# Kernel tuning notes

Hardware: AMD Instinct MI355X
Metric: run time of the kernel (lower is better)

The kernel has to match this reference:

```python
import jax, jax.numpy as jnp
import numpy as np
from jax import lax

# shifts generated by _generate_shifts(kernel_size=3): (s1, s2) pairs with
# (s1, s2) >= (0, 0) lexicographically, excluding (0, 0)
SHIFTS = [(0, 1), (1, -1), (1, 0), (1, 1)]


def conv2d_same(x, w, b):
    # x: (B, C_in, H, W), w: (C_out, C_in, kH, kW), b: (C_out,)
    y = lax.conv_general_dilated(
        x, w, window_strides=(1, 1), padding='SAME',
        dimension_numbers=('NCHW', 'OIHW', 'NCHW'))
    return y + b[None, :, None, None]


def setup_inputs() -> dict:
    key = jax.random.key(0)
    k1, k2, k3, k4, k5 = jax.random.split(key, 5)
    B, C_in, C_out, H, W, K = 8, 64, 64, 256, 256, 3
    fan = C_in * K * K
    return {
        'x': jax.random.normal(k1, (B, C_in, H, W), dtype=jnp.float32),
        'w1': jax.random.normal(k2, (C_out, C_in, K, K), dtype=jnp.float32) / np.sqrt(fan),
        'b1': jax.random.normal(k3, (C_out,), dtype=jnp.float32) * 0.01,
        'w2': jax.random.normal(k4, (C_out, C_in, K, K), dtype=jnp.float32) / np.sqrt(fan),
        'b2': jax.random.normal(k5, (C_out,), dtype=jnp.float32) * 0.01,
    }


def reference(x, w1, b1, w2, b2):
    linear_term = conv2d_same(x, w1, b1)
    # torch.roll(x, shifts=(shift_y, shift_x), dims=(2,3)) with
    # circular_shift(x, s1, s2) -> shift_x=s1, shift_y=s2.
    # conv2 is linear, so sum_i conv2(prod_i) == conv2(sum_i prod_i)
    # with the bias added once per shift.
    quad_in = jnp.zeros_like(x)
    for s1, s2 in SHIFTS:
        x_shifted = jnp.roll(x, shift=(s2, s1), axis=(2, 3))
        quad_in = quad_in + jnp.clip(x * x_shifted, -1.0, 1.0)
    quadratic_term = conv2d_same(quad_in, w2, b2 * float(len(SHIFTS)))
    return linear_term + quadratic_term
```

## Files before the change

### kernel.cpp

```cpp
#include <hip/hip_runtime.h>
#include <stdint.h>


typedef short s16x8 __attribute__((ext_vector_type(8)));
typedef float f32x4 __attribute__((ext_vector_type(4)));

__device__ __forceinline__ float clip1(float v) { return fminf(fmaxf(v, -1.f), 1.f); }

__device__ __forceinline__ unsigned short f2bf(float f) {
    union { float f; unsigned u; } v; v.f = f;
    unsigned u = v.u;
    return (unsigned short)((u + 0x7fffu + ((u >> 16) & 1u)) >> 16);
}

__device__ __forceinline__ float bf2f(unsigned short u) {
    union { unsigned v; float f; } t; t.v = ((unsigned)u) << 16; return t.f;
}

__global__ void prep_w(const float* __restrict__ w1, const float* __restrict__ w2,
                       unsigned short* __restrict__ Wb) {
    int idx = blockIdx.x * 256 + threadIdx.x;
    int kk = idx % 96;
    int rest = idx / 96;
    int co = rest & 63; rest >>= 6;
    int cc = rest & 3;
    int kh = rest >> 2;
    int kw = kk >> 5;
    int cci = kk & 31;
    int c2 = cc * 32 + cci;
    const float* src = (c2 < 64) ? w1 : w2;
    int ci = c2 & 63;
    Wb[idx] = f2bf(src[((co * 64 + ci) * 3 + kh) * 3 + kw]);
}

__global__ __launch_bounds__(512, 1) void prep_u2(const float* __restrict__ x,
                                                  unsigned short* __restrict__ U) {
    __shared__ unsigned short X[3][64][268];
    int bid = blockIdx.x;
    int bh = ((bid & 7) << 8) + (bid >> 3);
    int b = bh >> 8, h = bh & 255;
    int tid = threadIdx.x;

    for (int it = 0; it < 24; ++it) {
        int idx = tid + (it << 9);
        int w4 = idx & 63;
        int c  = (idx >> 6) & 63;
        int r  = idx >> 12;
        int gr = (h + r + 255) & 255;
        const float4 v = *(const float4*)(x + (((size_t)(b * 64 + c)) << 16)
                                            + (gr << 8) + (w4 << 2));
        ushort4 p;
        p.x = f2bf(v.x); p.y = f2bf(v.y); p.z = f2bf(v.z); p.w = f2bf(v.w);
        *(ushort4*)&X[r][c][w4 << 2] = p;
    }
    __syncthreads();

    int c  = tid & 63;
    int wv = tid >> 6;
    int p0 = wv << 5;
    int pm0 = (p0 + 255) & 255;
    float pxc = bf2f(X[1][c][pm0]);
    float pxu = bf2f(X[0][c][pm0]);
    float pxd = bf2f(X[2][c][pm0]);
    size_t base = ((size_t)bh) << 8;
#pragma unroll 4
    for (int i = 0; i < 32; ++i) {
        int p = p0 + i;
        unsigned short xcb = X[1][c][p];
        float xc = bf2f(xcb);
        float xu = bf2f(X[0][c][p]);
        float xd = bf2f(X[2][c][p]);
        float q = clip1(xc * xu) + clip1(xc * pxd) + clip1(xc * pxc) + clip1(xc * pxu);
        size_t po = (base + p) << 7;
        U[po + c]      = xcb;
        U[po + 64 + c] = f2bf(q);
        pxc = xc; pxu = xu; pxd = xd;
    }
}

__global__ __launch_bounds__(512, 4) void conv5(
        const unsigned short* __restrict__ U,
        const unsigned short* __restrict__ Wb,
        const float* __restrict__ b1, const float* __restrict__ b2,
        float* __restrict__ out) {
    __shared__ unsigned short Alds[3][64][104];
    __shared__ unsigned short Ib[2][130][40];

    int bid = blockIdx.x;
    int logical = ((bid & 7) << 7) + (bid >> 3);
    int b = logical >> 7;
    int rem = logical & 127;
    int h0 = (rem >> 1) << 2;
    int whalf = rem & 1;
    int w0 = whalf << 7;
    int tid = threadIdx.x;
    int wid = tid >> 6;
    int ln = tid & 63;
    int lr = ln & 15;
    int lq = ln >> 4;
    int rowsel = wid >> 1;
    int pq = wid & 1;
    int o = h0 + rowsel;

    f32x4 acc[4][4];
#pragma unroll
    for (int m = 0; m < 4; m++)
#pragma unroll
        for (int n = 0; n < 4; n++) {
            acc[m][n][0] = 0.f; acc[m][n][1] = 0.f; acc[m][n][2] = 0.f; acc[m][n][3] = 0.f;
        }

    const size_t ubase = ((size_t)b) << 23;

    int cur = 0;
    for (int cc = 0; cc < 4; cc++) {
        for (int i = tid; i < 2304; i += 512) {
            int kh = i / 768;
            int remw = i - kh * 768;
            int co = remw / 12;
            int kk = (remw - co * 12) << 3;
            *(uint4*)&Alds[kh][co][kk] =
                *(const uint4*)&Wb[(((size_t)((kh * 4 + cc) * 64 + co)) * 96) + kk];
        }
        {
            int r = h0 - 1;
            if (r >= 0) {
                const unsigned short* usrc = U + ubase + (((size_t)r) << 15) + cc * 32;
                for (int i = tid; i < 520; i += 512) {
                    int p = i >> 2, q = i & 3;
                    int gcol = w0 + p - 1;
                    uint4 v = (gcol < 0 || gcol > 255) ? make_uint4(0u, 0u, 0u, 0u)
                              : *(const uint4*)&usrc[(((size_t)gcol) << 7) + q * 8];
                    *(uint4*)&Ib[cur][p][q * 8] = v;
                }
            }
        }
        __syncthreads();

        for (int j = 0; j < 6; j++) {
            int rn = h0 + j;
            bool have = (j < 5) && (rn <= 255);
            uint4 s0;
            if (have) {
                const unsigned short* usrc = U + ubase + (((size_t)rn) << 15) + cc * 32;
                int p = tid >> 2, q = tid & 3;
                int gcol = w0 + p - 1;
                s0 = (gcol < 0 || gcol > 255) ? make_uint4(0u, 0u, 0u, 0u)
                     : *(const uint4*)&usrc[(((size_t)gcol) << 7) + q * 8];
            }
            int r = h0 - 1 + j;
            int kh = j - rowsel;
            if (kh >= 0 && kh <= 2 && r >= 0 && r <= 255) {
                __builtin_amdgcn_s_setprio(1);
#pragma unroll
                for (int kw = 0; kw < 3; kw++) {
                    s16x8 af[4], bfr[4];
#pragma unroll
                    for (int m = 0; m < 4; m++)
                        af[m] = *(const s16x8*)&Alds[kh][m * 16 + lr][kw * 32 + lq * 8];
#pragma unroll
                    for (int n = 0; n < 4; n++)
                        bfr[n] = *(const s16x8*)&Ib[cur][(pq << 6) + n * 16 + lr + kw][lq * 8];
#pragma unroll
                    for (int m = 0; m < 4; m++)
#pragma unroll
                        for (int n = 0; n < 4; n++)
                            acc[m][n] = __builtin_amdgcn_mfma_f32_16x16x32_bf16(af[m], bfr[n], acc[m][n], 0, 0, 0);
                }
                __builtin_amdgcn_s_setprio(0);
            }
            if (have) {
                { int p = tid >> 2, q = tid & 3; *(uint4*)&Ib[cur ^ 1][p][q * 8] = s0; }
                if (tid < 8) {
                    int i2 = tid + 512;
                    int p = i2 >> 2, q = i2 & 3;
                    int gcol = w0 + p - 1;
                    const unsigned short* usrc = U + ubase + (((size_t)rn) << 15) + cc * 32;
                    uint4 v = (gcol < 0 || gcol > 255) ? make_uint4(0u, 0u, 0u, 0u)
                              : *(const uint4*)&usrc[(((size_t)gcol) << 7) + q * 8];
                    *(uint4*)&Ib[cur ^ 1][p][q * 8] = v;
                }
            }
            __syncthreads();
            if (j < 5) cur ^= 1;
        }
    }

#pragma unroll
    for (int m = 0; m < 4; m++) {
#pragma unroll
        for (int jj = 0; jj < 4; jj++) {
            int co = m * 16 + lq * 4 + jj;
            float bias = b1[co] + 4.f * b2[co];
#pragma unroll
            for (int n = 0; n < 4; n++) {
                int wpix = w0 + (pq << 6) + n * 16 + lr;
                out[(((size_t)(b * 64 + co)) << 16) + (o << 8) + wpix] = acc[m][n][jj] + bias;
            }
        }
    }
}

__global__ void fallback_conv(const float* __restrict__ x,
                              const float* __restrict__ w1, const float* __restrict__ b1,
                              const float* __restrict__ w2, const float* __restrict__ b2,
                              float* __restrict__ out) {
    size_t idx = (size_t)blockIdx.x * 256 + threadIdx.x;
    int w = idx & 255;
    int h = (int)(idx >> 8) & 255;
    int co = (int)(idx >> 16) & 63;
    int b = (int)(idx >> 22);
    float acc = b1[co] + 4.f * b2[co];
    const float* xb = x + (((size_t)b * 64) << 16);
    for (int ci = 0; ci < 64; ci++) {
        const float* xp = xb + (((size_t)ci) << 16);
        for (int kh = 0; kh < 3; kh++) {
            int hh = h + kh - 1;
            if (hh < 0 || hh > 255) continue;
            for (int kw = 0; kw < 3; kw++) {
                int ww = w + kw - 1;
                if (ww < 0 || ww > 255) continue;
                float xv = xp[(hh << 8) + ww];
                float g1 = w1[((co * 64 + ci) * 3 + kh) * 3 + kw];
                float g2 = w2[((co * 64 + ci) * 3 + kh) * 3 + kw];
                int hm = (hh + 255) & 255, hp = (hh + 1) & 255, wm = (ww + 255) & 255;
                float q = clip1(xv * xp[(hm << 8) + ww]) + clip1(xv * xp[(hp << 8) + wm])
                        + clip1(xv * xp[(hh << 8) + wm]) + clip1(xv * xp[(hm << 8) + wm]);
                acc = fmaf(g1, xv, acc);
                acc = fmaf(g2, q, acc);
            }
        }
    }
    out[idx] = acc;
}

extern "C" void kernel_launch(void* const* d_in, const int* in_sizes, int n_in,
                              void* d_out, int out_size, void* d_ws, size_t ws_size,
                              hipStream_t stream) {
    const float* x  = (const float*)d_in[0];
    const float* w1 = (const float*)d_in[1];
    const float* b1 = (const float*)d_in[2];
    const float* w2 = (const float*)d_in[3];
    const float* b2 = (const float*)d_in[4];
    float* out = (float*)d_out;

    const size_t WB_BYTES = 262144;
    const size_t U_BYTES  = (size_t)8 * 256 * 256 * 128 * 2;
    if (ws_size >= WB_BYTES + U_BYTES) {
        unsigned short* Wb = (unsigned short*)d_ws;
        unsigned short* U  = (unsigned short*)((char*)d_ws + WB_BYTES);
        prep_w<<<dim3(288), dim3(256), 0, stream>>>(w1, w2, Wb);
        prep_u2<<<dim3(2048), dim3(512), 0, stream>>>(x, U);
        conv5<<<dim3(1024), dim3(512), 0, stream>>>(U, Wb, b1, b2, out);
    } else {
        fallback_conv<<<dim3(131072), dim3(256), 0, stream>>>(x, w1, b1, w2, b2, out);
    }
}
```

Before: 165.0 us.

## Stage whole 6-row input tile per channel chunk via direct global-to-LDS loads

After: 174.3 us. 1.06x slower.

```diff
diff --git a/kernel.cpp b/kernel.cpp
--- a/kernel.cpp
+++ b/kernel.cpp
@@ -15,6 +15,12 @@
 
 __device__ __forceinline__ float bf2f(unsigned short u) {
     union { unsigned v; float f; } t; t.v = ((unsigned)u) << 16; return t.f;
+}
+
+__device__ __forceinline__ void gload16(const void* g, void* l) {
+    __builtin_amdgcn_global_load_lds(
+        (const __attribute__((address_space(1))) unsigned int*)g,
+        (__attribute__((address_space(3))) unsigned int*)l, 16, 0, 0);
 }
 
 __global__ void prep_w(const float* __restrict__ w1, const float* __restrict__ w2,
@@ -78,13 +84,13 @@
     }
 }
 
-__global__ __launch_bounds__(512, 4) void conv5(
+__global__ __launch_bounds__(512, 2) void conv6(
         const unsigned short* __restrict__ U,
         const unsigned short* __restrict__ Wb,
         const float* __restrict__ b1, const float* __restrict__ b2,
         float* __restrict__ out) {
-    __shared__ unsigned short Alds[3][64][104];
-    __shared__ unsigned short Ib[2][130][40];
+    __shared__ unsigned short Alds[3][64][96];
+    __shared__ unsigned short Ib[2][6][130][32];
 
     int bid = blockIdx.x;
     int logical = ((bid & 7) << 7) + (bid >> 3);
@@ -102,6 +108,8 @@
     int pq = wid & 1;
     int o = h0 + rowsel;
 
+    const size_t ubase = ((size_t)b) << 23;
+
     f32x4 acc[4][4];
 #pragma unroll
     for (int m = 0; m < 4; m++)
@@ -110,79 +118,88 @@
             acc[m][n][0] = 0.f; acc[m][n][1] = 0.f; acc[m][n][2] = 0.f; acc[m][n][3] = 0.f;
         }
 
-    const size_t ubase = ((size_t)b) << 23;
+    auto stage_input = [&](int ccx, int nb) {
+        const unsigned short* ub = U + ubase + ccx * 32;
+#pragma unroll
+        for (int ir = 0; ir < 6; ++ir) {
+            int r = h0 - 1 + ir;
+            if (r < 0 || r > 255) continue;
+            int p = 1 + (tid >> 2), q = tid & 3;
+            const unsigned short* g = ub + (((size_t)r) << 15)
+                                        + (((size_t)(w0 + p - 1)) << 7) + q * 8;
+            unsigned short* l = &Ib[nb][ir][1][0] + (size_t)wid * 512;
+            gload16(g, l);
+        }
+    };
+    auto stage_weights = [&](int ccx) {
+#pragma unroll
+        for (int k = 0; k < 5; ++k) {
+            int J = k * 512 + tid;
+            if (J < 2304) {
+                int kh = J / 768;
+                int remw = J - kh * 768;
+                const unsigned short* g = Wb + (size_t)(kh * 4 + ccx) * 6144 + remw * 8;
+                unsigned short* l = ((unsigned short*)Alds) + (size_t)(k * 512 + wid * 64) * 8;
+                gload16(g, l);
+            }
+        }
+    };
+    auto fix_edges = [&](int ccx, int nb) {
+        if (tid < 48) {
+            int ir = tid >> 3, rest = tid & 7;
+            int side = rest >> 2, q = rest & 3;
+            int p = side ? 129 : 0;
+            int gcol = side ? (w0 + 128) : (w0 - 1);
+            int r = h0 - 1 + ir;
+            uint4 v = make_uint4(0u, 0u, 0u, 0u);
+            if (gcol >= 0 && gcol <= 255 && r >= 0 && r <= 255)
+                v = *(const uint4*)(U + ubase + (((size_t)r) << 15)
+                                    + (((size_t)gcol) << 7) + ccx * 32 + q * 8);
+            *(uint4*)&Ib[nb][ir][p][q * 8] = v;
+        }
+        if (h0 == 0)
+            for (int i = tid; i < 520; i += 512)
+                *(uint4*)&Ib[nb][0][i >> 2][(i & 3) * 8] = make_uint4(0u, 0u, 0u, 0u);
+        if (h0 == 252)
+            for (int i = tid; i < 520; i += 512)
+                *(uint4*)&Ib[nb][5][i >> 2][(i & 3) * 8] = make_uint4(0u, 0u, 0u, 0u);
+    };
+
+    stage_input(0, 0);
+    stage_weights(0);
+    fix_edges(0, 0);
+    __syncthreads();
 
     int cur = 0;
-    for (int cc = 0; cc < 4; cc++) {
-        for (int i = tid; i < 2304; i += 512) {
-            int kh = i / 768;
-            int remw = i - kh * 768;
-            int co = remw / 12;
-            int kk = (remw - co * 12) << 3;
-            *(uint4*)&Alds[kh][co][kk] =
-                *(const uint4*)&Wb[(((size_t)((kh * 4 + cc) * 64 + co)) * 96) + kk];
-        }
-        {
-            int r = h0 - 1;
-            if (r >= 0) {
-                const unsigned short* usrc = U + ubase + (((size_t)r) << 15) + cc * 32;
-                for (int i = tid; i < 520; i += 512) {
-                    int p = i >> 2, q = i & 3;
-                    int gcol = w0 + p - 1;
-                    uint4 v = (gcol < 0 || gcol > 255) ? make_uint4(0u, 0u, 0u, 0u)
-                              : *(const uint4*)&usrc[(((size_t)gcol) << 7) + q * 8];
-                    *(uint4*)&Ib[cur][p][q * 8] = v;
-                }
-            }
-        }
+    for (int cc = 0; cc < 4; ++cc) {
+        if (cc < 3) stage_input(cc + 1, cur ^ 1);
+        __builtin_amdgcn_s_setprio(1);
+#pragma unroll
+        for (int kh = 0; kh < 3; ++kh) {
+            int ir = rowsel + kh;
+#pragma unroll
+            for (int kw = 0; kw < 3; ++kw) {
+                s16x8 af[4], bfr[4];
+#pragma unroll
+                for (int m = 0; m < 4; m++)
+                    af[m] = *(const s16x8*)&Alds[kh][m * 16 + lr][kw * 32 + lq * 8];
+#pragma unroll
+                for (int n = 0; n < 4; n++)
+                    bfr[n] = *(const s16x8*)&Ib[cur][ir][(pq << 6) + n * 16 + lr + kw][lq * 8];
+#pragma unroll
+                for (int m = 0; m < 4; m++)
+#pragma unroll
+                    for (int n = 0; n < 4; n++)
+                        acc[m][n] = __builtin_amdgcn_mfma_f32_16x16x32_bf16(af[m], bfr[n], acc[m][n], 0, 0, 0);
+            }
+        }
+        __builtin_amdgcn_s_setprio(0);
         __syncthreads();
-
-        for (int j = 0; j < 6; j++) {
-            int rn = h0 + j;
-            bool have = (j < 5) && (rn <= 255);
-            uint4 s0;
-            if (have) {
-                const unsigned short* usrc = U + ubase + (((size_t)rn) << 15) + cc * 32;
-                int p = tid >> 2, q = tid & 3;
-                int gcol = w0 + p - 1;
-                s0 = (gcol < 0 || gcol > 255) ? make_uint4(0u, 0u, 0u, 0u)
-                     : *(const uint4*)&usrc[(((size_t)gcol) << 7) + q * 8];
-            }
-            int r = h0 - 1 + j;
-            int kh = j - rowsel;
-            if (kh >= 0 && kh <= 2 && r >= 0 && r <= 255) {
-                __builtin_amdgcn_s_setprio(1);
-#pragma unroll
-                for (int kw = 0; kw < 3; kw++) {
-                    s16x8 af[4], bfr[4];
-#pragma unroll
-                    for (int m = 0; m < 4; m++)
-                        af[m] = *(const s16x8*)&Alds[kh][m * 16 + lr][kw * 32 + lq * 8];
-#pragma unroll
-                    for (int n = 0; n < 4; n++)
-                        bfr[n] = *(const s16x8*)&Ib[cur][(pq << 6) + n * 16 + lr + kw][lq * 8];
-#pragma unroll
-                    for (int m = 0; m < 4; m++)
-#pragma unroll
-                        for (int n = 0; n < 4; n++)
-                            acc[m][n] = __builtin_amdgcn_mfma_f32_16x16x32_bf16(af[m], bfr[n], acc[m][n], 0, 0, 0);
-                }
-                __builtin_amdgcn_s_setprio(0);
-            }
-            if (have) {
-                { int p = tid >> 2, q = tid & 3; *(uint4*)&Ib[cur ^ 1][p][q * 8] = s0; }
-                if (tid < 8) {
-                    int i2 = tid + 512;
-                    int p = i2 >> 2, q = i2 & 3;
-                    int gcol = w0 + p - 1;
-                    const unsigned short* usrc = U + ubase + (((size_t)rn) << 15) + cc * 32;
-                    uint4 v = (gcol < 0 || gcol > 255) ? make_uint4(0u, 0u, 0u, 0u)
-                              : *(const uint4*)&usrc[(((size_t)gcol) << 7) + q * 8];
-                    *(uint4*)&Ib[cur ^ 1][p][q * 8] = v;
-                }
-            }
+        if (cc < 3) {
+            stage_weights(cc + 1);
+            fix_edges(cc + 1, cur ^ 1);
             __syncthreads();
-            if (j < 5) cur ^= 1;
+            cur ^= 1;
         }
     }
 
@@ -251,7 +268,7 @@
         unsigned short* U  = (unsigned short*)((char*)d_ws + WB_BYTES);
         prep_w<<<dim3(288), dim3(256), 0, stream>>>(w1, w2, Wb);
         prep_u2<<<dim3(2048), dim3(512), 0, stream>>>(x, U);
-        conv5<<<dim3(1024), dim3(512), 0, stream>>>(U, Wb, b1, b2, out);
+        conv6<<<dim3(1024), dim3(512), 0, stream>>>(U, Wb, b1, b2, out);
     } else {
         fallback_conv<<<dim3(131072), dim3(256), 0, stream>>>(x, w1, b1, w2, b2, out);
     }
```
